# Optimization experiments

Hardware: AMD Instinct MI355X
Metric: run time of the kernel (lower is better)

## Reference

```python
import jax, jax.numpy as jnp
import numpy as np

N, E, D_IN, HID, HEADS, TS_OUT = 100000, 200000, 165, 64, 8, 5
HD1 = HID // HEADS  # 8 per-head channels in layer 1
HD2 = HID           # 64 per-head channels in layer 2 (concat=False -> mean)


def _glorot(key, shape):
    fan_in, fan_out = shape[0], shape[1]
    s = np.sqrt(6.0 / (fan_in + fan_out)).astype(np.float32)
    return jax.random.uniform(key, shape, jnp.float32, -s, s)


def setup_inputs() -> dict:
    key = jax.random.key(0)
    ks = jax.random.split(key, 24)
    inp = {
        "x": jax.random.normal(ks[0], (N, D_IN), jnp.float32),
        "edge_index": jax.random.randint(ks[1], (2, E), 0, N, jnp.int32),
        "timestamp_target": jax.random.randint(ks[2], (N,), 0, TS_OUT, jnp.int32),
        "node_target": jax.random.randint(ks[3], (N,), 0, 2, jnp.int32),
        "node_mask": jax.random.randint(ks[4], (N,), 0, 2, jnp.int32).astype(jnp.bool_),
        # GATConv layer 1: in=165 -> 8 heads x 8 ch, concat -> 64
        "W1": _glorot(ks[5], (D_IN, HEADS * HD1)),
        "att_src1": _glorot(ks[6], (HEADS, HD1)),
        "att_dst1": _glorot(ks[7], (HEADS, HD1)),
        "b1": jnp.zeros((HEADS * HD1,), jnp.float32),
        # GATConv layer 2: in=64 -> 8 heads x 64 ch, mean -> 64
        "W2": _glorot(ks[8], (HID, HEADS * HD2)),
        "att_src2": _glorot(ks[9], (HEADS, HD2)),
        "att_dst2": _glorot(ks[10], (HEADS, HD2)),
        "b2": jnp.zeros((HD2,), jnp.float32),
        # timestamp predictor MLP
        "ts_w1": _glorot(ks[11], (HID, HID)), "ts_b1": jnp.zeros((HID,), jnp.float32),
        "ts_w2": _glorot(ks[12], (HID, TS_OUT)), "ts_b2": jnp.zeros((TS_OUT,), jnp.float32),
        # class predictor MLP
        "cls_w1": _glorot(ks[13], (HID, HID)), "cls_b1": jnp.zeros((HID,), jnp.float32),
        "cls_w2": _glorot(ks[14], (HID, 2)), "cls_b2": jnp.zeros((2,), jnp.float32),
    }
    return inp


def _gat_layer(x, src, dst, n, W, a_src, a_dst, b, concat):
    H, C = a_src.shape
    h = (x @ W).reshape(n, H, C)                      # [N,H,C]
    a_s = (h * a_src).sum(-1)                         # [N,H]
    a_d = (h * a_dst).sum(-1)                         # [N,H]
    alpha = jax.nn.leaky_relu(a_s[src] + a_d[dst], 0.2)   # [E,H]
    amax = jax.ops.segment_max(alpha, dst, num_segments=n)
    ea = jnp.exp(alpha - amax[dst])
    denom = jax.ops.segment_sum(ea, dst, num_segments=n)
    a = ea / (denom[dst] + 1e-16)                     # segment softmax over incoming edges
    out = jax.ops.segment_sum(h[src] * a[:, :, None], dst, num_segments=n)  # [N,H,C]
    out = out.reshape(n, H * C) if concat else out.mean(axis=1)
    return out + b


def _ce(logits, targets):
    lp = jax.nn.log_softmax(logits, axis=-1)
    return -jnp.take_along_axis(lp, targets[:, None].astype(jnp.int32), axis=1)[:, 0]


def reference(x, edge_index, timestamp_target, node_target, node_mask,
              W1, att_src1, att_dst1, b1, W2, att_src2, att_dst2, b2,
              ts_w1, ts_b1, ts_w2, ts_b2, cls_w1, cls_b1, cls_w2, cls_b2):
    n = x.shape[0]
    loops = jnp.arange(n, dtype=edge_index.dtype)
    src = jnp.concatenate([edge_index[0], loops])     # add self loops (PyG default)
    dst = jnp.concatenate([edge_index[1], loops])
    h = _gat_layer(x, src, dst, n, W1, att_src1, att_dst1, b1, True)   # [N,64]
    h = _gat_layer(h, src, dst, n, W2, att_src2, att_dst2, b2, False)  # [N,64]
    # gradient reversal is identity in the forward pass
    ts_pred = jax.nn.relu(h @ ts_w1 + ts_b1) @ ts_w2 + ts_b2           # [N,5]
    cls_pred = jax.nn.relu(h @ cls_w1 + cls_b1) @ cls_w2 + cls_b2      # [N,2]
    ts_loss = _ce(ts_pred, timestamp_target).mean()
    m = node_mask.astype(jnp.float32)
    cls_loss = (_ce(cls_pred, node_target) * m).sum() / m.sum()
    return cls_loss + 1.0 * ts_loss
```

## Files before the change

kernel.cpp:

```cpp
#include <hip/hip_runtime.h>
#include <hip/hip_bf16.h>

#define NN 100000
#define NE 200000
#define NT (NE + NN)
#define DIN 165
#define PREPB 128
#define INITB 391
#define PACKB 32
#define W1PB 24
#define MISCGRID (PREPB + INITB + PACKB + W1PB)
#define NODEB 1563
#define XDW ((size_t)NN * DIN)
#define G1ROWS 32
#define G1NDMA 21

typedef __attribute__((ext_vector_type(8))) short bf16x8_t;
typedef __attribute__((ext_vector_type(4))) float f32x4_t;
typedef _Float16 h2_t __attribute__((ext_vector_type(2)));
typedef _Float16 f16x8_t __attribute__((ext_vector_type(8)));

#define AS1 __attribute__((address_space(1)))
#define AS3 __attribute__((address_space(3)))

static __device__ __forceinline__ unsigned short f2bf(float f) {
    __hip_bfloat16 b = __float2bfloat16(f);
    return *(unsigned short*)&b;
}
static __device__ __forceinline__ float bfu(unsigned short u) {
    __hip_bfloat16 b = *(__hip_bfloat16*)&u;
    return __bfloat162float(b);
}
static __device__ __forceinline__ unsigned pkh2(float a, float b) {
    h2_t v; v[0] = (_Float16)a; v[1] = (_Float16)b;
    return *(unsigned*)&v;
}


__global__ __launch_bounds__(256) void k_misc(const float* W2, const float* a2s, const float* a2d,
                                              float* wsd, __hip_bfloat16* W2pT,
                                              int* cnt, int* fill,
                                              const float* tsw1, const float* cw1,
                                              __hip_bfloat16* wB,
                                              const float* W1, unsigned* W1pT, float* zbuf) {
    int b = blockIdx.x;
    int tid = threadIdx.x;
    if (b < PREPB) {
        int i = b * 256 + tid;
        int c = i >> 9, j = i & 511;
        int hh = j >> 6, kk = j & 63;
        W2pT[i] = __float2bfloat16(W2[kk * 512 + hh * 64 + c]);
        if (b == 0) zbuf[tid] = 0.f;
        if (i < 512) {
            int h = i >> 6, k = i & 63;
            float s = 0.f, d = 0.f;
            for (int cc = 0; cc < 64; cc++) {
                float w = W2[k * 512 + h * 64 + cc];
                s += w * a2s[h * 64 + cc];
                d += w * a2d[h * 64 + cc];
            }
            wsd[i] = s; wsd[512 + i] = d;
        }
    } else if (b < PREPB + INITB) {
        int i = (b - PREPB) * 256 + tid;
        if (i < NN) { cnt[i] = 0; fill[i] = 0; }
    } else if (b < PREPB + INITB + PACKB) {
        int i = (b - PREPB - INITB) * 256 + tid;
        if (i < 8192) {
            int c = i >> 6, k = i & 63;
            float v = (c < 64) ? tsw1[k * 64 + c] : cw1[k * 64 + (c - 64)];
            wB[i] = __float2bfloat16(v);
        }
    } else {
        int i = (b - PREPB - INITB - PACKB) * 256 + tid;
        if (i < 6144) {
            int c = i / 96, kp = i - c * 96;
            int k = 2 * kp;
            float f0 = (k < DIN) ? W1[k * 64 + c] : 0.f;
            float f1 = (k + 1 < DIN) ? W1[(k + 1) * 64 + c] : 0.f;
            W1pT[i] = pkh2(f0, f1);
        }
    }
}


__global__ __launch_bounds__(256) void k_count(const int* dstE, int* cnt) {
    int e = blockIdx.x * 256 + threadIdx.x;
    if (e < NE) atomicAdd(&cnt[dstE[e]], 1);
}

__global__ __launch_bounds__(256) void k_scanA(const int* cnt, int* rowptr, int* bsum) {
    __shared__ int sm[256];
    int t = threadIdx.x;
    int base = blockIdx.x * 1024;
    int v[4]; int s = 0;
    for (int i = 0; i < 4; i++) {
        int idx = base + t * 4 + i;
        v[i] = (idx < NN) ? (cnt[idx] + 1) : 0;
        s += v[i];
    }
    sm[t] = s; __syncthreads();
    for (int off = 1; off < 256; off <<= 1) {
        int x = (t >= off) ? sm[t - off] : 0;
        __syncthreads();
        sm[t] += x;
        __syncthreads();
    }
    int run = sm[t] - s;
    for (int i = 0; i < 4; i++) {
        run += v[i];
        int idx = base + t * 4 + i;
        if (idx < NN) rowptr[idx + 1] = run;
    }
    if (t == 255) bsum[blockIdx.x] = sm[255];
}

__global__ __launch_bounds__(64) void k_scanB(int* bsum, int nb) {
    int lane = threadIdx.x;
    int v0 = (lane < nb) ? bsum[lane] : 0;
    int v1 = (64 + lane < nb) ? bsum[64 + lane] : 0;
    int s0 = v0;
    for (int off = 1; off < 64; off <<= 1) { int t = __shfl_up(s0, off); if (lane >= off) s0 += t; }
    int tot0 = __shfl(s0, 63);
    int s1 = v1;
    for (int off = 1; off < 64; off <<= 1) { int t = __shfl_up(s1, off); if (lane >= off) s1 += t; }
    if (lane < nb) bsum[lane] = s0 - v0;
    if (64 + lane < nb) bsum[64 + lane] = tot0 + s1 - v1;
}

__global__ __launch_bounds__(256) void k_scanC(const int* bsum, int* rowptr) {
    int i = blockIdx.x * 256 + threadIdx.x;
    if (i < NN) rowptr[i + 1] += bsum[i >> 10];
    if (i == 0) rowptr[0] = 0;
}

__global__ __launch_bounds__(256) void k_fill(const int* srcE, const int* dstE,
                                              const int* rowptr, int* fill, int* col, int* rowv) {
    int i = blockIdx.x * 256 + threadIdx.x;
    if (i >= NT) return;
    int s, d;
    if (i < NE) { s = srcE[i]; d = dstE[i]; }
    else        { s = i - NE; d = s; }
    int p = rowptr[d] + atomicAdd(&fill[d], 1);
    col[p] = s;
    rowv[p] = d;
}


__global__ __launch_bounds__(128) void k_gemm1(const float* x, const unsigned* W1pT,
                                               const float* att_s, const float* att_d,
                                               const float* zsrc,
                                               __hip_bfloat16* h1b, float* aad1) {
    __shared__ float X[G1NDMA * 256];
    int tid = threadIdx.x;
    int l = tid & 63, w = tid >> 6;
    int n0 = blockIdx.x * G1ROWS;
    int frow = l & 15, kg = l >> 4;

    size_t tb = (size_t)n0 * DIN;
    for (int i = w; i < G1NDMA; i += 2) {
        size_t gd = tb + (size_t)i * 256 + (size_t)l * 4;
        const float* g = (gd + 4 <= XDW) ? (x + gd) : (zsrc + l * 4);
        __builtin_amdgcn_global_load_lds((const AS1 float*)g,
                                         (AS3 float*)(X + i * 256), 16, 0, 0);
    }
    uint4 B[6][4];
    #pragma unroll
    for (int s = 0; s < 6; s++)
        #pragma unroll
        for (int t = 0; t < 4; t++)
            B[s][t] = *(const uint4*)&W1pT[(t * 16 + frow) * 96 + s * 16 + kg * 4];
    __syncthreads();

    f32x4_t acc[4] = {};
    int rbase = (w * 16 + frow) * DIN + kg * 8;
    #pragma unroll
    for (int s = 0; s < 6; s++) {
        f16x8_t av;
        #pragma unroll
        for (int j = 0; j < 8; j++) av[j] = (_Float16)X[rbase + s * 32 + j];
        #pragma unroll
        for (int t = 0; t < 4; t++)
            acc[t] = __builtin_amdgcn_mfma_f32_16x16x32_f16(av, *(f16x8_t*)&B[s][t], acc[t], 0, 0, 0);
    }

    int nw = n0 + w * 16;
    float asv[4], adv[4];
    #pragma unroll
    for (int t = 0; t < 4; t++) {
        int c = t * 16 + frow;
        asv[t] = att_s[c]; adv[t] = att_d[c];
    }
    int hb = (l >> 3) & 1;
    #pragma unroll
    for (int q = 0; q < 4; q++) {
        int n = nw + kg * 4 + q;
        #pragma unroll
        for (int t = 0; t < 4; t++) {
            float sv = acc[t][q] * asv[t];
            float dv = acc[t][q] * adv[t];
            sv += __shfl_xor(sv, 1); sv += __shfl_xor(sv, 2); sv += __shfl_xor(sv, 4);
            dv += __shfl_xor(dv, 1); dv += __shfl_xor(dv, 2); dv += __shfl_xor(dv, 4);
            if ((l & 7) == 0) {
                int h = t * 2 + hb;
                aad1[(size_t)n * 16 + h]     = sv;
                aad1[(size_t)n * 16 + 8 + h] = dv;
            }
        }
    }

    __syncthreads();
    unsigned short* Hw = (unsigned short*)X + w * 1152;
    #pragma unroll
    for (int t = 0; t < 4; t++)
        #pragma unroll
        for (int q = 0; q < 4; q++)
            Hw[(kg * 4 + q) * 72 + t * 16 + frow] = f2bf(acc[t][q]);
    int rr = l >> 2, cc = l & 3;
    int n2 = nw + rr;
    unsigned short* dst = (unsigned short*)h1b + (size_t)n2 * 64 + cc * 16;
    *(uint4*)dst       = *(const uint4*)&Hw[rr * 72 + cc * 16];
    *(uint4*)(dst + 8) = *(const uint4*)&Hw[rr * 72 + cc * 16 + 8];
}


__global__ __launch_bounds__(256) void k_edgew(const float* aad, const int* col, const int* rowv,
                                               __hip_bfloat16* web) {
    int e = blockIdx.x * 256 + threadIdx.x;
    if (e >= NT) return;
    int s = col[e], d = rowv[e];
    float4 s0 = *(const float4*)&aad[(size_t)s * 16];
    float4 s1 = *(const float4*)&aad[(size_t)s * 16 + 4];
    float4 dd0 = *(const float4*)&aad[(size_t)d * 16 + 8];
    float4 dd1 = *(const float4*)&aad[(size_t)d * 16 + 12];
    float as[8] = {s0.x, s0.y, s0.z, s0.w, s1.x, s1.y, s1.z, s1.w};
    float ad[8] = {dd0.x, dd0.y, dd0.z, dd0.w, dd1.x, dd1.y, dd1.z, dd1.w};
    unsigned p[4];
    #pragma unroll
    for (int q = 0; q < 4; q++) {
        float a0 = as[2*q]   + ad[2*q];
        float a1 = as[2*q+1] + ad[2*q+1];
        a0 = a0 > 0.f ? a0 : 0.2f * a0;
        a1 = a1 > 0.f ? a1 : 0.2f * a1;
        p[q] = (unsigned)f2bf(__expf(a0)) | ((unsigned)f2bf(__expf(a1)) << 16);
    }
    *(uint4*)&web[(size_t)e * 8] = make_uint4(p[0], p[1], p[2], p[3]);
}


__global__ __launch_bounds__(256) void k_agg1f(const __hip_bfloat16* h1b, const __hip_bfloat16* we1b,
                                               const int* rowptr, const int* col,
                                               const float* b1, const float* wsd,
                                               __hip_bfloat16* out1b, float* aad2) {
    int tid = threadIdx.x;
    int q8 = tid & 7;
    int n = blockIdx.x * 32 + (tid >> 3);
    const unsigned short* h1u = (const unsigned short*)h1b;
    const unsigned short* weu = (const unsigned short*)we1b;
    int rs = rowptr[n], re = rowptr[n + 1];
    float acc[8] = {};
    float den = 0.f;
    for (int eb = rs; eb < re; eb += 4) {
        int c4[4];
        #pragma unroll
        for (int j = 0; j < 4; j++) c4[j] = col[min(eb + j, re - 1)];
        #pragma unroll
        for (int j = 0; j < 4; j++) {
            int e = min(eb + j, re - 1);
            float w = bfu(weu[(size_t)e * 8 + q8]);
            w = (eb + j < re) ? w : 0.f;
            uint4 hv = *(const uint4*)&h1u[(size_t)c4[j] * 64 + q8 * 8];
            den += w;
            acc[0] += w * bfu((unsigned short)(hv.x & 0xffff));
            acc[1] += w * bfu((unsigned short)(hv.x >> 16));
            acc[2] += w * bfu((unsigned short)(hv.y & 0xffff));
            acc[3] += w * bfu((unsigned short)(hv.y >> 16));
            acc[4] += w * bfu((unsigned short)(hv.z & 0xffff));
            acc[5] += w * bfu((unsigned short)(hv.z >> 16));
            acc[6] += w * bfu((unsigned short)(hv.w & 0xffff));
            acc[7] += w * bfu((unsigned short)(hv.w >> 16));
        }
    }
    float inv = 1.0f / (den + 1e-16f);
    float4 b0 = *(const float4*)&b1[q8 * 8];
    float4 b4 = *(const float4*)&b1[q8 * 8 + 4];
    float bb[8] = {b0.x, b0.y, b0.z, b0.w, b4.x, b4.y, b4.z, b4.w};
    unsigned short u[8];
    float r[8];
    #pragma unroll
    for (int k = 0; k < 8; k++) {
        u[k] = f2bf(acc[k] * inv + bb[k]);
        r[k] = bfu(u[k]);
    }
    unsigned short* ou = (unsigned short*)out1b;
    uint4 pk;
    pk.x = (unsigned)u[0] | ((unsigned)u[1] << 16);
    pk.y = (unsigned)u[2] | ((unsigned)u[3] << 16);
    pk.z = (unsigned)u[4] | ((unsigned)u[5] << 16);
    pk.w = (unsigned)u[6] | ((unsigned)u[7] << 16);
    *(uint4*)&ou[(size_t)n * 64 + q8 * 8] = pk;

    float p[16];
    #pragma unroll
    for (int j = 0; j < 16; j++) {
        float4 w0 = *(const float4*)&wsd[j * 64 + q8 * 8];
        float4 w4 = *(const float4*)&wsd[j * 64 + q8 * 8 + 4];
        p[j] = r[0] * w0.x + r[1] * w0.y + r[2] * w0.z + r[3] * w0.w
             + r[4] * w4.x + r[5] * w4.y + r[6] * w4.z + r[7] * w4.w;
    }
    #pragma unroll
    for (int s = 1; s < 8; s <<= 1)
        #pragma unroll
        for (int j = 0; j < 16; j++) p[j] += __shfl_xor(p[j], s);
    float p0 = 0.f, p1 = 0.f;
    #pragma unroll
    for (int j = 0; j < 8; j++) {
        p0 = (q8 == j) ? p[j] : p0;
        p1 = (q8 == j) ? p[8 + j] : p1;
    }
    aad2[(size_t)n * 16 + q8]     = p0;
    aad2[(size_t)n * 16 + 8 + q8] = p1;
}


__global__ __launch_bounds__(256) void k_l2f(const __hip_bfloat16* out1b, const __hip_bfloat16* we2b,
                                             const int* rowptr, const int* col,
                                             const __hip_bfloat16* W2pT, const float* b2,
                                             const __hip_bfloat16* wB,
                                             const float* tsb1, const float* cb1,
                                             const float* tsw2, const float* tsb2,
                                             const float* cw2, const float* cb2,
                                             const int* tst, const int* ctg, const unsigned char* msk,
                                             float* part) {
    __shared__ unsigned short Ax[64 * 512];
    __shared__ unsigned short Bl[64 * 72];
    __shared__ float red[4][3];
    int tid = threadIdx.x;
    int l = tid & 63, w = tid >> 6;
    int n0 = blockIdx.x * 64;
    int frow = l & 15, kg = l >> 4;

    const unsigned short* o1u = (const unsigned short*)out1b;
    const unsigned short* weu = (const unsigned short*)we2b;
    int q8 = tid & 7;
    #pragma unroll 1
    for (int pass = 0; pass < 2; pass++) {
        int j = pass * 32 + (tid >> 3);
        int n = n0 + j;
        int rs = 0, re = 0;
        if (n < NN) { rs = rowptr[n]; re = rowptr[n + 1]; }
        float acc[8][8];
        float den[8];
        #pragma unroll
        for (int h = 0; h < 8; h++) {
            den[h] = 0.f;
            #pragma unroll
            for (int c = 0; c < 8; c++) acc[h][c] = 0.f;
        }
        for (int eb = rs; eb < re; eb += 4) {
            int c4[4];
            #pragma unroll
            for (int jj = 0; jj < 4; jj++) c4[jj] = col[min(eb + jj, re - 1)];
            #pragma unroll
            for (int jj = 0; jj < 4; jj++) {
                int e = min(eb + jj, re - 1);
                uint4 wv = *(const uint4*)&weu[(size_t)e * 8];
                uint4 hv = *(const uint4*)&o1u[(size_t)c4[jj] * 64 + q8 * 8];
                float vm = (eb + jj < re) ? 1.f : 0.f;
                float hc[8] = {bfu((unsigned short)(hv.x & 0xffff)), bfu((unsigned short)(hv.x >> 16)),
                               bfu((unsigned short)(hv.y & 0xffff)), bfu((unsigned short)(hv.y >> 16)),
                               bfu((unsigned short)(hv.z & 0xffff)), bfu((unsigned short)(hv.z >> 16)),
                               bfu((unsigned short)(hv.w & 0xffff)), bfu((unsigned short)(hv.w >> 16))};
                float wt[8] = {bfu((unsigned short)(wv.x & 0xffff)), bfu((unsigned short)(wv.x >> 16)),
                               bfu((unsigned short)(wv.y & 0xffff)), bfu((unsigned short)(wv.y >> 16)),
                               bfu((unsigned short)(wv.z & 0xffff)), bfu((unsigned short)(wv.z >> 16)),
                               bfu((unsigned short)(wv.w & 0xffff)), bfu((unsigned short)(wv.w >> 16))};
                #pragma unroll
                for (int h = 0; h < 8; h++) {
                    float ww = wt[h] * vm;
                    den[h] += ww;
                    #pragma unroll
                    for (int c = 0; c < 8; c++) acc[h][c] += ww * hc[c];
                }
            }
        }
        unsigned short* row = &Ax[j * 512];
        #pragma unroll
        for (int h = 0; h < 8; h++) {
            float inv = 1.0f / (den[h] + 1e-16f);
            uint4 pk;
            pk.x = (unsigned)f2bf(acc[h][0] * inv) | ((unsigned)f2bf(acc[h][1] * inv) << 16);
            pk.y = (unsigned)f2bf(acc[h][2] * inv) | ((unsigned)f2bf(acc[h][3] * inv) << 16);
            pk.z = (unsigned)f2bf(acc[h][4] * inv) | ((unsigned)f2bf(acc[h][5] * inv) << 16);
            pk.w = (unsigned)f2bf(acc[h][6] * inv) | ((unsigned)f2bf(acc[h][7] * inv) << 16);
            int blk = (h * 8 + q8) ^ (j & 7);
            *(uint4*)&row[blk * 8] = pk;
        }
    }
    __syncthreads();

    const unsigned short* B_g = (const unsigned short*)W2pT;
    f32x4_t gacc[4] = {};
    #pragma unroll 1
    for (int k0 = 0; k0 < 512; k0 += 64) {
        #pragma unroll
        for (int ll = 0; ll < 2; ll++) {
            int u = tid + ll * 256;
            int r = u >> 3, seg = u & 7;
            *(uint4*)&Bl[r * 72 + seg * 8] = *(const uint4*)&B_g[(size_t)r * 512 + k0 + seg * 8];
        }
        __syncthreads();
        #pragma unroll
        for (int kk = 0; kk < 2; kk++) {
            int blk = ((k0 >> 3) + kk * 4 + kg) ^ (frow & 7);
            bf16x8_t a = *(const bf16x8_t*)&Ax[(w * 16 + frow) * 512 + blk * 8];
            #pragma unroll
            for (int t = 0; t < 4; t++) {
                bf16x8_t bb = *(const bf16x8_t*)&Bl[(t * 16 + frow) * 72 + kk * 32 + kg * 8];
                gacc[t] = __builtin_amdgcn_mfma_f32_16x16x32_bf16(a, bb, gacc[t], 0, 0, 0);
            }
        }
        __syncthreads();
    }

    unsigned short* o2L = Ax;
    #pragma unroll
    for (int t = 0; t < 4; t++) {
        float bias = b2[t * 16 + frow];
        #pragma unroll
        for (int q = 0; q < 4; q++)
            o2L[(w * 16 + kg * 4 + q) * 72 + t * 16 + frow] = f2bf(0.125f * gacc[t][q] + bias);
    }
    __syncthreads();
    const unsigned short* wBu = (const unsigned short*)wB;
    f32x4_t a2c[8] = {};
    #pragma unroll
    for (int kk = 0; kk < 2; kk++) {
        bf16x8_t a2 = *(const bf16x8_t*)&o2L[(w * 16 + frow) * 72 + kk * 32 + kg * 8];
        #pragma unroll
        for (int t2 = 0; t2 < 8; t2++) {
            bf16x8_t b2f = *(const bf16x8_t*)&wBu[(t2 * 16 + frow) * 64 + kk * 32 + kg * 8];
            a2c[t2] = __builtin_amdgcn_mfma_f32_16x16x32_bf16(a2, b2f, a2c[t2], 0, 0, 0);
        }
    }

    float lg[4][5]; float lc[4][2];
    #pragma unroll
    for (int q = 0; q < 4; q++) {
        #pragma unroll
        for (int t = 0; t < 5; t++) lg[q][t] = 0.f;
        lc[q][0] = 0.f; lc[q][1] = 0.f;
    }
    #pragma unroll
    for (int t2 = 0; t2 < 4; t2++) {
        int c = t2 * 16 + frow;
        float bb = tsb1[c];
        float w0 = tsw2[c * 5 + 0], w1 = tsw2[c * 5 + 1], w2 = tsw2[c * 5 + 2],
              w3 = tsw2[c * 5 + 3], w4 = tsw2[c * 5 + 4];
        #pragma unroll
        for (int q = 0; q < 4; q++) {
            float v = fmaxf(a2c[t2][q] + bb, 0.f);
            lg[q][0] += v * w0; lg[q][1] += v * w1; lg[q][2] += v * w2;
            lg[q][3] += v * w3; lg[q][4] += v * w4;
        }
    }
    #pragma unroll
    for (int t2 = 0; t2 < 4; t2++) {
        int c = t2 * 16 + frow;
        float bb = cb1[c];
        float u0 = cw2[c * 2], u1 = cw2[c * 2 + 1];
        #pragma unroll
        for (int q = 0; q < 4; q++) {
            float v = fmaxf(a2c[t2 + 4][q] + bb, 0.f);
            lc[q][0] += v * u0; lc[q][1] += v * u1;
        }
    }
    #pragma unroll
    for (int q = 0; q < 4; q++) {
        #pragma unroll
        for (int t = 0; t < 5; t++) {
            lg[q][t] += __shfl_xor(lg[q][t], 1);
            lg[q][t] += __shfl_xor(lg[q][t], 2);
            lg[q][t] += __shfl_xor(lg[q][t], 4);
            lg[q][t] += __shfl_xor(lg[q][t], 8);
        }
        #pragma unroll
        for (int t = 0; t < 2; t++) {
            lc[q][t] += __shfl_xor(lc[q][t], 1);
            lc[q][t] += __shfl_xor(lc[q][t], 2);
            lc[q][t] += __shfl_xor(lc[q][t], 4);
            lc[q][t] += __shfl_xor(lc[q][t], 8);
        }
    }
    float tsl = 0.f, cll = 0.f, mval = 0.f;
    if (frow == 0) {
        #pragma unroll
        for (int q = 0; q < 4; q++) {
            int n = n0 + w * 16 + kg * 4 + q;
            if (n < NN) {
                float L[5];
                #pragma unroll
                for (int t = 0; t < 5; t++) L[t] = lg[q][t] + tsb2[t];
                float mx = fmaxf(fmaxf(fmaxf(L[0], L[1]), fmaxf(L[2], L[3])), L[4]);
                float se = 0.f;
                #pragma unroll
                for (int t = 0; t < 5; t++) se += __expf(L[t] - mx);
                int tg = tst[n];
                float pick = 0.f;
                #pragma unroll
                for (int t = 0; t < 5; t++) pick += (t == tg) ? L[t] : 0.f;
                tsl += mx + __logf(se) - pick;
                float C0 = lc[q][0] + cb2[0];
                float C1 = lc[q][1] + cb2[1];
                float mx2 = fmaxf(C0, C1);
                float lse2 = mx2 + __logf(__expf(C0 - mx2) + __expf(C1 - mx2));
                float mv = msk[n] ? 1.f : 0.f;
                float pick2 = ctg[n] ? C1 : C0;
                cll += (lse2 - pick2) * mv;
                mval += mv;
            }
        }
    }
    #pragma unroll
    for (int off = 1; off < 64; off <<= 1) {
        tsl  += __shfl_xor(tsl, off);
        cll  += __shfl_xor(cll, off);
        mval += __shfl_xor(mval, off);
    }
    if (l == 0) { red[w][0] = tsl; red[w][1] = cll; red[w][2] = mval; }
    __syncthreads();
    if (tid == 0) {
        part[blockIdx.x * 3 + 0] = red[0][0] + red[1][0] + red[2][0] + red[3][0];
        part[blockIdx.x * 3 + 1] = red[0][1] + red[1][1] + red[2][1] + red[3][1];
        part[blockIdx.x * 3 + 2] = red[0][2] + red[1][2] + red[2][2] + red[3][2];
    }
}

__global__ __launch_bounds__(256) void k_final(const float* part, float* out, int nb) {
    __shared__ float sm[3][256];
    int tid = threadIdx.x;
    float a = 0, b = 0, c = 0;
    for (int i = tid; i < nb; i += 256) { a += part[i*3]; b += part[i*3+1]; c += part[i*3+2]; }
    sm[0][tid] = a; sm[1][tid] = b; sm[2][tid] = c;
    __syncthreads();
    for (int s = 128; s > 0; s >>= 1) {
        if (tid < s) {
            sm[0][tid] += sm[0][tid + s];
            sm[1][tid] += sm[1][tid + s];
            sm[2][tid] += sm[2][tid + s];
        }
        __syncthreads();
    }
    if (tid == 0) out[0] = sm[1][0] / sm[2][0] + sm[0][0] / (float)NN;
}


extern "C" void kernel_launch(void* const* d_in, const int* in_sizes, int n_in,
                              void* d_out, int out_size, void* d_ws, size_t ws_size,
                              hipStream_t stream) {
    const float* x    = (const float*)d_in[0];
    const int*   ei   = (const int*)d_in[1];
    const int*   tst  = (const int*)d_in[2];
    const int*   ctg  = (const int*)d_in[3];
    const unsigned char* msk = (const unsigned char*)d_in[4];
    const float* W1   = (const float*)d_in[5];
    const float* a1s  = (const float*)d_in[6];
    const float* a1d  = (const float*)d_in[7];
    const float* b1   = (const float*)d_in[8];
    const float* W2   = (const float*)d_in[9];
    const float* a2s  = (const float*)d_in[10];
    const float* a2d  = (const float*)d_in[11];
    const float* b2   = (const float*)d_in[12];
    const float* tsw1 = (const float*)d_in[13];
    const float* tsb1 = (const float*)d_in[14];
    const float* tsw2 = (const float*)d_in[15];
    const float* tsb2 = (const float*)d_in[16];
    const float* cw1  = (const float*)d_in[17];
    const float* cb1  = (const float*)d_in[18];
    const float* cw2  = (const float*)d_in[19];
    const float* cb2  = (const float*)d_in[20];
    const int* srcE = ei;
    const int* dstE = ei + NE;

    char* ws = (char*)d_ws;
    size_t off = 0;
    auto alloc = [&](size_t b) { size_t o = off; off = (off + b + 255) & ~(size_t)255; return o; };
    int*   cnt    = (int*)(ws + alloc((size_t)NN * 4));
    int*   fill   = (int*)(ws + alloc((size_t)NN * 4));
    int*   rowptr = (int*)(ws + alloc((size_t)(NN + 1) * 4));
    int*   bsum   = (int*)(ws + alloc(128 * 4));
    int*   col    = (int*)(ws + alloc((size_t)NT * 4));
    int*   rowv   = (int*)(ws + alloc((size_t)NT * 4));
    float* aad1   = (float*)(ws + alloc((size_t)NN * 16 * 4));
    __hip_bfloat16* out1b = (__hip_bfloat16*)(ws + alloc((size_t)NN * 64 * 2));
    float* aad2   = (float*)(ws + alloc((size_t)NN * 16 * 4));
    float* wsd    = (float*)(ws + alloc(1024 * 4));
    __hip_bfloat16* W2pT  = (__hip_bfloat16*)(ws + alloc(32768 * 2));
    __hip_bfloat16* wB    = (__hip_bfloat16*)(ws + alloc(8192 * 2));
    unsigned* W1pT = (unsigned*)(ws + alloc(6144 * 4));
    float* zbuf   = (float*)(ws + alloc(256 * 4));
    __hip_bfloat16* h1b   = (__hip_bfloat16*)(ws + alloc((size_t)NN * 64 * 2));
    __hip_bfloat16* web   = (__hip_bfloat16*)(ws + alloc((size_t)NT * 8 * 2));
    float* part   = (float*)(ws + alloc((size_t)NODEB * 3 * 4));
    (void)ws_size; (void)in_sizes; (void)n_in; (void)out_size;

    int nb_scan = (NN + 1023) / 1024;

    k_misc<<<MISCGRID, 256, 0, stream>>>(W2, a2s, a2d, wsd, W2pT, cnt, fill,
                                         tsw1, cw1, wB, W1, W1pT, zbuf);
    k_count<<<(NE + 255) / 256, 256, 0, stream>>>(dstE, cnt);
    k_scanA<<<nb_scan, 256, 0, stream>>>(cnt, rowptr, bsum);
    k_scanB<<<1, 64, 0, stream>>>(bsum, nb_scan);
    k_scanC<<<(NN + 255) / 256, 256, 0, stream>>>(bsum, rowptr);
    k_fill<<<(NT + 255) / 256, 256, 0, stream>>>(srcE, dstE, rowptr, fill, col, rowv);

    k_gemm1<<<NN / G1ROWS, 128, 0, stream>>>(x, W1pT, a1s, a1d, zbuf, h1b, aad1);
    k_edgew<<<(NT + 255) / 256, 256, 0, stream>>>(aad1, col, rowv, web);
    k_agg1f<<<NN / 32, 256, 0, stream>>>(h1b, web, rowptr, col, b1, wsd, out1b, aad2);
    k_edgew<<<(NT + 255) / 256, 256, 0, stream>>>(aad2, col, rowv, web);

    k_l2f<<<NODEB, 256, 0, stream>>>(out1b, web, rowptr, col, W2pT, b2, wB,
                                     tsb1, cb1, tsw2, tsb2, cw2, cb2, tst, ctg, msk, part);

    k_final<<<1, 256, 0, stream>>>(part, (float*)d_out, NODEB);
}
```

Measured before the change: 177.7 us.

## Fuse edge-weight computation into aggregation kernels and drop scan and final launches

Removes the two k_edgew passes and computes the leaky-relu/exp attention weights inline inside both aggregation kernels, reading per-node attention scalars from aad instead of a materialized per-edge bf16 weight array. The weights are now fp32 rather than bf16-rounded. Merges k_scanB into k_scanC, where every block recomputes the block prefix in shared memory, and replaces k_final with atomic accumulation plus a last-block-done finish in k_l2f. This cuts four launches and the per-edge weight write/read traffic, at the cost of redundant exp work per lane and wave shuffles in layer 2.

```diff
diff --git a/kernel.cpp b/kernel.cpp
--- a/kernel.cpp
+++ b/kernel.cpp
@@ -42,7 +42,8 @@
                                               int* cnt, int* fill,
                                               const float* tsw1, const float* cw1,
                                               __hip_bfloat16* wB,
-                                              const float* W1, unsigned* W1pT, float* zbuf) {
+                                              const float* W1, unsigned* W1pT, float* zbuf,
+                                              float* acc3, int* cnt1) {
     int b = blockIdx.x;
     int tid = threadIdx.x;
     if (b < PREPB) {
@@ -51,6 +52,7 @@
         int hh = j >> 6, kk = j & 63;
         W2pT[i] = __float2bfloat16(W2[kk * 512 + hh * 64 + c]);
         if (b == 0) zbuf[tid] = 0.f;
+        if (b == 0 && tid == 0) { acc3[0] = 0.f; acc3[1] = 0.f; acc3[2] = 0.f; cnt1[0] = 0; }
         if (i < 512) {
             int h = i >> 6, k = i & 63;
             float s = 0.f, d = 0.f;
@@ -115,22 +117,24 @@
     if (t == 255) bsum[blockIdx.x] = sm[255];
 }
 
-__global__ __launch_bounds__(64) void k_scanB(int* bsum, int nb) {
-    int lane = threadIdx.x;
-    int v0 = (lane < nb) ? bsum[lane] : 0;
-    int v1 = (64 + lane < nb) ? bsum[64 + lane] : 0;
-    int s0 = v0;
-    for (int off = 1; off < 64; off <<= 1) { int t = __shfl_up(s0, off); if (lane >= off) s0 += t; }
-    int tot0 = __shfl(s0, 63);
-    int s1 = v1;
-    for (int off = 1; off < 64; off <<= 1) { int t = __shfl_up(s1, off); if (lane >= off) s1 += t; }
-    if (lane < nb) bsum[lane] = s0 - v0;
-    if (64 + lane < nb) bsum[64 + lane] = tot0 + s1 - v1;
-}
-
-__global__ __launch_bounds__(256) void k_scanC(const int* bsum, int* rowptr) {
-    int i = blockIdx.x * 256 + threadIdx.x;
-    if (i < NN) rowptr[i + 1] += bsum[i >> 10];
+__global__ __launch_bounds__(256) void k_scanC(const int* bsum, int* rowptr, int nb) {
+    __shared__ int pre[128];
+    int tid = threadIdx.x;
+    if (tid < 64) {
+        int lane = tid;
+        int v0 = (lane < nb) ? bsum[lane] : 0;
+        int v1 = (64 + lane < nb) ? bsum[64 + lane] : 0;
+        int s0 = v0;
+        for (int off = 1; off < 64; off <<= 1) { int t = __shfl_up(s0, off); if (lane >= off) s0 += t; }
+        int tot0 = __shfl(s0, 63);
+        int s1 = v1;
+        for (int off = 1; off < 64; off <<= 1) { int t = __shfl_up(s1, off); if (lane >= off) s1 += t; }
+        pre[lane] = s0 - v0;
+        pre[64 + lane] = tot0 + s1 - v1;
+    }
+    __syncthreads();
+    int i = blockIdx.x * 256 + tid;
+    if (i < NN) rowptr[i + 1] += pre[i >> 10];
     if (i == 0) rowptr[0] = 0;
 }
 
@@ -224,31 +228,7 @@
 }
 
 
-__global__ __launch_bounds__(256) void k_edgew(const float* aad, const int* col, const int* rowv,
-                                               __hip_bfloat16* web) {
-    int e = blockIdx.x * 256 + threadIdx.x;
-    if (e >= NT) return;
-    int s = col[e], d = rowv[e];
-    float4 s0 = *(const float4*)&aad[(size_t)s * 16];
-    float4 s1 = *(const float4*)&aad[(size_t)s * 16 + 4];
-    float4 dd0 = *(const float4*)&aad[(size_t)d * 16 + 8];
-    float4 dd1 = *(const float4*)&aad[(size_t)d * 16 + 12];
-    float as[8] = {s0.x, s0.y, s0.z, s0.w, s1.x, s1.y, s1.z, s1.w};
-    float ad[8] = {dd0.x, dd0.y, dd0.z, dd0.w, dd1.x, dd1.y, dd1.z, dd1.w};
-    unsigned p[4];
-    #pragma unroll
-    for (int q = 0; q < 4; q++) {
-        float a0 = as[2*q]   + ad[2*q];
-        float a1 = as[2*q+1] + ad[2*q+1];
-        a0 = a0 > 0.f ? a0 : 0.2f * a0;
-        a1 = a1 > 0.f ? a1 : 0.2f * a1;
-        p[q] = (unsigned)f2bf(__expf(a0)) | ((unsigned)f2bf(__expf(a1)) << 16);
-    }
-    *(uint4*)&web[(size_t)e * 8] = make_uint4(p[0], p[1], p[2], p[3]);
-}
-
-
-__global__ __launch_bounds__(256) void k_agg1f(const __hip_bfloat16* h1b, const __hip_bfloat16* we1b,
+__global__ __launch_bounds__(256) void k_agg1f(const __hip_bfloat16* h1b, const float* aad1,
                                                const int* rowptr, const int* col,
                                                const float* b1, const float* wsd,
                                                __hip_bfloat16* out1b, float* aad2) {
@@ -256,7 +236,7 @@
     int q8 = tid & 7;
     int n = blockIdx.x * 32 + (tid >> 3);
     const unsigned short* h1u = (const unsigned short*)h1b;
-    const unsigned short* weu = (const unsigned short*)we1b;
+    float ad_own = aad1[(size_t)n * 16 + 8 + q8];
     int rs = rowptr[n], re = rowptr[n + 1];
     float acc[8] = {};
     float den = 0.f;
@@ -264,12 +244,19 @@
         int c4[4];
         #pragma unroll
         for (int j = 0; j < 4; j++) c4[j] = col[min(eb + j, re - 1)];
+        float asv[4]; uint4 hv4[4];
         #pragma unroll
         for (int j = 0; j < 4; j++) {
-            int e = min(eb + j, re - 1);
-            float w = bfu(weu[(size_t)e * 8 + q8]);
+            asv[j] = aad1[(size_t)c4[j] * 16 + q8];
+            hv4[j] = *(const uint4*)&h1u[(size_t)c4[j] * 64 + q8 * 8];
+        }
+        #pragma unroll
+        for (int j = 0; j < 4; j++) {
+            float a = asv[j] + ad_own;
+            a = a > 0.f ? a : 0.2f * a;
+            float w = __expf(a);
             w = (eb + j < re) ? w : 0.f;
-            uint4 hv = *(const uint4*)&h1u[(size_t)c4[j] * 64 + q8 * 8];
+            uint4 hv = hv4[j];
             den += w;
             acc[0] += w * bfu((unsigned short)(hv.x & 0xffff));
             acc[1] += w * bfu((unsigned short)(hv.x >> 16));
@@ -323,7 +310,7 @@
 }
 
 
-__global__ __launch_bounds__(256) void k_l2f(const __hip_bfloat16* out1b, const __hip_bfloat16* we2b,
+__global__ __launch_bounds__(256) void k_l2f(const __hip_bfloat16* out1b, const float* aad2,
                                              const int* rowptr, const int* col,
                                              const __hip_bfloat16* W2pT, const float* b2,
                                              const __hip_bfloat16* wB,
@@ -331,7 +318,7 @@
                                              const float* tsw2, const float* tsb2,
                                              const float* cw2, const float* cb2,
                                              const int* tst, const int* ctg, const unsigned char* msk,
-                                             float* part) {
+                                             float* acc3, int* cnt1, float* out) {
     __shared__ unsigned short Ax[64 * 512];
     __shared__ unsigned short Bl[64 * 72];
     __shared__ float red[4][3];
@@ -341,14 +328,18 @@
     int frow = l & 15, kg = l >> 4;
 
     const unsigned short* o1u = (const unsigned short*)out1b;
-    const unsigned short* weu = (const unsigned short*)we2b;
     int q8 = tid & 7;
+    int base8 = l & 56;
     #pragma unroll 1
     for (int pass = 0; pass < 2; pass++) {
         int j = pass * 32 + (tid >> 3);
         int n = n0 + j;
         int rs = 0, re = 0;
-        if (n < NN) { rs = rowptr[n]; re = rowptr[n + 1]; }
+        float ad_own = 0.f;
+        if (n < NN) {
+            rs = rowptr[n]; re = rowptr[n + 1];
+            ad_own = aad2[(size_t)n * 16 + 8 + q8];
+        }
         float acc[8][8];
         float den[8];
         #pragma unroll
@@ -361,26 +352,31 @@
             int c4[4];
             #pragma unroll
             for (int jj = 0; jj < 4; jj++) c4[jj] = col[min(eb + jj, re - 1)];
+            float asv[4]; uint4 hv4[4];
             #pragma unroll
             for (int jj = 0; jj < 4; jj++) {
-                int e = min(eb + jj, re - 1);
-                uint4 wv = *(const uint4*)&weu[(size_t)e * 8];
-                uint4 hv = *(const uint4*)&o1u[(size_t)c4[jj] * 64 + q8 * 8];
-                float vm = (eb + jj < re) ? 1.f : 0.f;
+                asv[jj] = aad2[(size_t)c4[jj] * 16 + q8];
+                hv4[jj] = *(const uint4*)&o1u[(size_t)c4[jj] * 64 + q8 * 8];
+            }
+            #pragma unroll
+            for (int jj = 0; jj < 4; jj++) {
+                float a = asv[jj] + ad_own;
+                a = a > 0.f ? a : 0.2f * a;
+                float wq = __expf(a);
+                wq = (eb + jj < re) ? wq : 0.f;
+                float wt[8];
+                #pragma unroll
+                for (int h = 0; h < 8; h++) wt[h] = __shfl(wq, base8 + h);
+                uint4 hv = hv4[jj];
                 float hc[8] = {bfu((unsigned short)(hv.x & 0xffff)), bfu((unsigned short)(hv.x >> 16)),
                                bfu((unsigned short)(hv.y & 0xffff)), bfu((unsigned short)(hv.y >> 16)),
                                bfu((unsigned short)(hv.z & 0xffff)), bfu((unsigned short)(hv.z >> 16)),
                                bfu((unsigned short)(hv.w & 0xffff)), bfu((unsigned short)(hv.w >> 16))};
-                float wt[8] = {bfu((unsigned short)(wv.x & 0xffff)), bfu((unsigned short)(wv.x >> 16)),
-                               bfu((unsigned short)(wv.y & 0xffff)), bfu((unsigned short)(wv.y >> 16)),
-                               bfu((unsigned short)(wv.z & 0xffff)), bfu((unsigned short)(wv.z >> 16)),
-                               bfu((unsigned short)(wv.w & 0xffff)), bfu((unsigned short)(wv.w >> 16))};
                 #pragma unroll
                 for (int h = 0; h < 8; h++) {
-                    float ww = wt[h] * vm;
-                    den[h] += ww;
+                    den[h] += wt[h];
                     #pragma unroll
-                    for (int c = 0; c < 8; c++) acc[h][c] += ww * hc[c];
+                    for (int c = 0; c < 8; c++) acc[h][c] += wt[h] * hc[c];
                 }
             }
         }
@@ -530,28 +526,21 @@
     if (l == 0) { red[w][0] = tsl; red[w][1] = cll; red[w][2] = mval; }
     __syncthreads();
     if (tid == 0) {
-        part[blockIdx.x * 3 + 0] = red[0][0] + red[1][0] + red[2][0] + red[3][0];
-        part[blockIdx.x * 3 + 1] = red[0][1] + red[1][1] + red[2][1] + red[3][1];
-        part[blockIdx.x * 3 + 2] = red[0][2] + red[1][2] + red[2][2] + red[3][2];
-    }
-}
-
-__global__ __launch_bounds__(256) void k_final(const float* part, float* out, int nb) {
-    __shared__ float sm[3][256];
-    int tid = threadIdx.x;
-    float a = 0, b = 0, c = 0;
-    for (int i = tid; i < nb; i += 256) { a += part[i*3]; b += part[i*3+1]; c += part[i*3+2]; }
-    sm[0][tid] = a; sm[1][tid] = b; sm[2][tid] = c;
-    __syncthreads();
-    for (int s = 128; s > 0; s >>= 1) {
-        if (tid < s) {
-            sm[0][tid] += sm[0][tid + s];
-            sm[1][tid] += sm[1][tid + s];
-            sm[2][tid] += sm[2][tid + s];
-        }
-        __syncthreads();
-    }
-    if (tid == 0) out[0] = sm[1][0] / sm[2][0] + sm[0][0] / (float)NN;
+        float s0 = red[0][0] + red[1][0] + red[2][0] + red[3][0];
+        float s1 = red[0][1] + red[1][1] + red[2][1] + red[3][1];
+        float s2 = red[0][2] + red[1][2] + red[2][2] + red[3][2];
+        atomicAdd(&acc3[0], s0);
+        atomicAdd(&acc3[1], s1);
+        atomicAdd(&acc3[2], s2);
+        __threadfence();
+        int old = atomicAdd(cnt1, 1);
+        if (old == NODEB - 1) {
+            float t0 = atomicAdd(&acc3[0], 0.f);
+            float t1 = atomicAdd(&acc3[1], 0.f);
+            float t2 = atomicAdd(&acc3[2], 0.f);
+            out[0] = t1 / t2 + t0 / (float)NN;
+        }
+    }
 }
 
 
@@ -600,27 +589,23 @@
     unsigned* W1pT = (unsigned*)(ws + alloc(6144 * 4));
     float* zbuf   = (float*)(ws + alloc(256 * 4));
     __hip_bfloat16* h1b   = (__hip_bfloat16*)(ws + alloc((size_t)NN * 64 * 2));
-    __hip_bfloat16* web   = (__hip_bfloat16*)(ws + alloc((size_t)NT * 8 * 2));
-    float* part   = (float*)(ws + alloc((size_t)NODEB * 3 * 4));
+    float* acc3   = (float*)(ws + alloc(4 * 4));
+    int*   cnt1   = (int*)(ws + alloc(4 * 4));
     (void)ws_size; (void)in_sizes; (void)n_in; (void)out_size;
 
     int nb_scan = (NN + 1023) / 1024;
 
     k_misc<<<MISCGRID, 256, 0, stream>>>(W2, a2s, a2d, wsd, W2pT, cnt, fill,
-                                         tsw1, cw1, wB, W1, W1pT, zbuf);
+                                         tsw1, cw1, wB, W1, W1pT, zbuf, acc3, cnt1);
     k_count<<<(NE + 255) / 256, 256, 0, stream>>>(dstE, cnt);
     k_scanA<<<nb_scan, 256, 0, stream>>>(cnt, rowptr, bsum);
-    k_scanB<<<1, 64, 0, stream>>>(bsum, nb_scan);
-    k_scanC<<<(NN + 255) / 256, 256, 0, stream>>>(bsum, rowptr);
+    k_scanC<<<(NN + 255) / 256, 256, 0, stream>>>(bsum, rowptr, nb_scan);
     k_fill<<<(NT + 255) / 256, 256, 0, stream>>>(srcE, dstE, rowptr, fill, col, rowv);
 
     k_gemm1<<<NN / G1ROWS, 128, 0, stream>>>(x, W1pT, a1s, a1d, zbuf, h1b, aad1);
-    k_edgew<<<(NT + 255) / 256, 256, 0, stream>>>(aad1, col, rowv, web);
-    k_agg1f<<<NN / 32, 256, 0, stream>>>(h1b, web, rowptr, col, b1, wsd, out1b, aad2);
-    k_edgew<<<(NT + 255) / 256, 256, 0, stream>>>(aad2, col, rowv, web);
-
-    k_l2f<<<NODEB, 256, 0, stream>>>(out1b, web, rowptr, col, W2pT, b2, wB,
-                                     tsb1, cb1, tsw2, tsb2, cw2, cb2, tst, ctg, msk, part);
-
-    k_final<<<1, 256, 0, stream>>>(part, (float*)d_out, NODEB);
-}
+    k_agg1f<<<NN / 32, 256, 0, stream>>>(h1b, aad1, rowptr, col, b1, wsd, out1b, aad2);
+
+    k_l2f<<<NODEB, 256, 0, stream>>>(out1b, aad2, rowptr, col, W2pT, b2, wB,
+                                     tsb1, cb1, tsw2, tsb2, cw2, cb2, tst, ctg, msk,
+                                     acc3, cnt1, (float*)d_out);
+}
```

Result: slower. 208.6 us (+17.4%).

## Halve layer-2 node tile, fold final reduction and scan into fewer launches

Applied to the files above, without the earlier changes.

The fused layer-2 kernel now handles 32 nodes per block instead of 64, with 3125 blocks, and its MFMA work is redistributed across the four waves (each wave takes a 16x32 output tile, and ts/cls heads are split between wave pairs). The separate final reduction kernel is replaced by atomic accumulation plus a last-block-done counter, and the block-sum scan kernel is merged into the scan-add kernel. This removes two kernel launches and the per-block serial two-pass loop, and the smaller LDS footprint should raise occupancy. The cost is float atomics with nondeterministic summation order and each scanC block redundantly scanning the block sums.

```diff
diff --git a/kernel.cpp b/kernel.cpp
--- a/kernel.cpp
+++ b/kernel.cpp
@@ -10,7 +10,7 @@
 #define PACKB 32
 #define W1PB 24
 #define MISCGRID (PREPB + INITB + PACKB + W1PB)
-#define NODEB 1563
+#define L2B 3125
 #define XDW ((size_t)NN * DIN)
 #define G1ROWS 32
 #define G1NDMA 21
@@ -42,7 +42,8 @@
                                               int* cnt, int* fill,
                                               const float* tsw1, const float* cw1,
                                               __hip_bfloat16* wB,
-                                              const float* W1, unsigned* W1pT, float* zbuf) {
+                                              const float* W1, unsigned* W1pT, float* zbuf,
+                                              float* acc3, int* cnt1) {
     int b = blockIdx.x;
     int tid = threadIdx.x;
     if (b < PREPB) {
@@ -51,6 +52,7 @@
         int hh = j >> 6, kk = j & 63;
         W2pT[i] = __float2bfloat16(W2[kk * 512 + hh * 64 + c]);
         if (b == 0) zbuf[tid] = 0.f;
+        if (b == 0 && tid == 0) { acc3[0] = 0.f; acc3[1] = 0.f; acc3[2] = 0.f; cnt1[0] = 0; }
         if (i < 512) {
             int h = i >> 6, k = i & 63;
             float s = 0.f, d = 0.f;
@@ -115,22 +117,24 @@
     if (t == 255) bsum[blockIdx.x] = sm[255];
 }
 
-__global__ __launch_bounds__(64) void k_scanB(int* bsum, int nb) {
-    int lane = threadIdx.x;
-    int v0 = (lane < nb) ? bsum[lane] : 0;
-    int v1 = (64 + lane < nb) ? bsum[64 + lane] : 0;
-    int s0 = v0;
-    for (int off = 1; off < 64; off <<= 1) { int t = __shfl_up(s0, off); if (lane >= off) s0 += t; }
-    int tot0 = __shfl(s0, 63);
-    int s1 = v1;
-    for (int off = 1; off < 64; off <<= 1) { int t = __shfl_up(s1, off); if (lane >= off) s1 += t; }
-    if (lane < nb) bsum[lane] = s0 - v0;
-    if (64 + lane < nb) bsum[64 + lane] = tot0 + s1 - v1;
-}
-
-__global__ __launch_bounds__(256) void k_scanC(const int* bsum, int* rowptr) {
-    int i = blockIdx.x * 256 + threadIdx.x;
-    if (i < NN) rowptr[i + 1] += bsum[i >> 10];
+__global__ __launch_bounds__(256) void k_scanC(const int* bsum, int* rowptr, int nb) {
+    __shared__ int pre[128];
+    int tid = threadIdx.x;
+    if (tid < 64) {
+        int lane = tid;
+        int v0 = (lane < nb) ? bsum[lane] : 0;
+        int v1 = (64 + lane < nb) ? bsum[64 + lane] : 0;
+        int s0 = v0;
+        for (int off = 1; off < 64; off <<= 1) { int t = __shfl_up(s0, off); if (lane >= off) s0 += t; }
+        int tot0 = __shfl(s0, 63);
+        int s1 = v1;
+        for (int off = 1; off < 64; off <<= 1) { int t = __shfl_up(s1, off); if (lane >= off) s1 += t; }
+        pre[lane] = s0 - v0;
+        pre[64 + lane] = tot0 + s1 - v1;
+    }
+    __syncthreads();
+    int i = blockIdx.x * 256 + tid;
+    if (i < NN) rowptr[i + 1] += pre[i >> 10];
     if (i == 0) rowptr[0] = 0;
 }
 
@@ -331,24 +335,22 @@
                                              const float* tsw2, const float* tsb2,
                                              const float* cw2, const float* cb2,
                                              const int* tst, const int* ctg, const unsigned char* msk,
-                                             float* part) {
-    __shared__ unsigned short Ax[64 * 512];
+                                             float* acc3, int* cnt1, float* out) {
+    __shared__ unsigned short Ax[32 * 512];
     __shared__ unsigned short Bl[64 * 72];
     __shared__ float red[4][3];
     int tid = threadIdx.x;
     int l = tid & 63, w = tid >> 6;
-    int n0 = blockIdx.x * 64;
+    int n0 = blockIdx.x * 32;
     int frow = l & 15, kg = l >> 4;
 
     const unsigned short* o1u = (const unsigned short*)out1b;
     const unsigned short* weu = (const unsigned short*)we2b;
     int q8 = tid & 7;
-    #pragma unroll 1
-    for (int pass = 0; pass < 2; pass++) {
-        int j = pass * 32 + (tid >> 3);
+    {
+        int j = tid >> 3;
         int n = n0 + j;
-        int rs = 0, re = 0;
-        if (n < NN) { rs = rowptr[n]; re = rowptr[n + 1]; }
+        int rs = rowptr[n], re = rowptr[n + 1];
         float acc[8][8];
         float den[8];
         #pragma unroll
@@ -400,7 +402,9 @@
     __syncthreads();
 
     const unsigned short* B_g = (const unsigned short*)W2pT;
-    f32x4_t gacc[4] = {};
+    int r0 = (w & 1) * 16;
+    int c0 = (w >> 1) * 32;
+    f32x4_t gacc[2] = {};
     #pragma unroll 1
     for (int k0 = 0; k0 < 512; k0 += 64) {
         #pragma unroll
@@ -413,10 +417,10 @@
         #pragma unroll
         for (int kk = 0; kk < 2; kk++) {
             int blk = ((k0 >> 3) + kk * 4 + kg) ^ (frow & 7);
-            bf16x8_t a = *(const bf16x8_t*)&Ax[(w * 16 + frow) * 512 + blk * 8];
-            #pragma unroll
-            for (int t = 0; t < 4; t++) {
-                bf16x8_t bb = *(const bf16x8_t*)&Bl[(t * 16 + frow) * 72 + kk * 32 + kg * 8];
+            bf16x8_t a = *(const bf16x8_t*)&Ax[(r0 + frow) * 512 + blk * 8];
+            #pragma unroll
+            for (int t = 0; t < 2; t++) {
+                bf16x8_t bb = *(const bf16x8_t*)&Bl[(c0 + t * 16 + frow) * 72 + kk * 32 + kg * 8];
                 gacc[t] = __builtin_amdgcn_mfma_f32_16x16x32_bf16(a, bb, gacc[t], 0, 0, 0);
             }
         }
@@ -425,79 +429,61 @@
 
     unsigned short* o2L = Ax;
     #pragma unroll
-    for (int t = 0; t < 4; t++) {
-        float bias = b2[t * 16 + frow];
+    for (int t = 0; t < 2; t++) {
+        float bias = b2[c0 + t * 16 + frow];
+        f32x4_t g = gacc[t];
         #pragma unroll
         for (int q = 0; q < 4; q++)
-            o2L[(w * 16 + kg * 4 + q) * 72 + t * 16 + frow] = f2bf(0.125f * gacc[t][q] + bias);
+            o2L[(r0 + kg * 4 + q) * 72 + c0 + t * 16 + frow] = f2bf(0.125f * g[q] + bias);
     }
     __syncthreads();
     const unsigned short* wBu = (const unsigned short*)wB;
-    f32x4_t a2c[8] = {};
+    int m0 = (w & 1) * 16;
+    int h0 = (w >> 1) * 64;
+    f32x4_t a2c[4] = {};
     #pragma unroll
     for (int kk = 0; kk < 2; kk++) {
-        bf16x8_t a2 = *(const bf16x8_t*)&o2L[(w * 16 + frow) * 72 + kk * 32 + kg * 8];
-        #pragma unroll
-        for (int t2 = 0; t2 < 8; t2++) {
-            bf16x8_t b2f = *(const bf16x8_t*)&wBu[(t2 * 16 + frow) * 64 + kk * 32 + kg * 8];
-            a2c[t2] = __builtin_amdgcn_mfma_f32_16x16x32_bf16(a2, b2f, a2c[t2], 0, 0, 0);
-        }
-    }
-
-    float lg[4][5]; float lc[4][2];
-    #pragma unroll
-    for (int q = 0; q < 4; q++) {
-        #pragma unroll
-        for (int t = 0; t < 5; t++) lg[q][t] = 0.f;
-        lc[q][0] = 0.f; lc[q][1] = 0.f;
-    }
-    #pragma unroll
-    for (int t2 = 0; t2 < 4; t2++) {
-        int c = t2 * 16 + frow;
-        float bb = tsb1[c];
-        float w0 = tsw2[c * 5 + 0], w1 = tsw2[c * 5 + 1], w2 = tsw2[c * 5 + 2],
-              w3 = tsw2[c * 5 + 3], w4 = tsw2[c * 5 + 4];
-        #pragma unroll
-        for (int q = 0; q < 4; q++) {
-            float v = fmaxf(a2c[t2][q] + bb, 0.f);
-            lg[q][0] += v * w0; lg[q][1] += v * w1; lg[q][2] += v * w2;
-            lg[q][3] += v * w3; lg[q][4] += v * w4;
-        }
-    }
-    #pragma unroll
-    for (int t2 = 0; t2 < 4; t2++) {
-        int c = t2 * 16 + frow;
-        float bb = cb1[c];
-        float u0 = cw2[c * 2], u1 = cw2[c * 2 + 1];
-        #pragma unroll
-        for (int q = 0; q < 4; q++) {
-            float v = fmaxf(a2c[t2 + 4][q] + bb, 0.f);
-            lc[q][0] += v * u0; lc[q][1] += v * u1;
-        }
-    }
-    #pragma unroll
-    for (int q = 0; q < 4; q++) {
-        #pragma unroll
-        for (int t = 0; t < 5; t++) {
-            lg[q][t] += __shfl_xor(lg[q][t], 1);
-            lg[q][t] += __shfl_xor(lg[q][t], 2);
-            lg[q][t] += __shfl_xor(lg[q][t], 4);
-            lg[q][t] += __shfl_xor(lg[q][t], 8);
-        }
-        #pragma unroll
-        for (int t = 0; t < 2; t++) {
-            lc[q][t] += __shfl_xor(lc[q][t], 1);
-            lc[q][t] += __shfl_xor(lc[q][t], 2);
-            lc[q][t] += __shfl_xor(lc[q][t], 4);
-            lc[q][t] += __shfl_xor(lc[q][t], 8);
-        }
-    }
+        bf16x8_t a2 = *(const bf16x8_t*)&o2L[(m0 + frow) * 72 + kk * 32 + kg * 8];
+        #pragma unroll
+        for (int t2 = 0; t2 < 4; t2++) {
+            bf16x8_t bf = *(const bf16x8_t*)&wBu[(h0 + t2 * 16 + frow) * 64 + kk * 32 + kg * 8];
+            a2c[t2] = __builtin_amdgcn_mfma_f32_16x16x32_bf16(a2, bf, a2c[t2], 0, 0, 0);
+        }
+    }
+
     float tsl = 0.f, cll = 0.f, mval = 0.f;
-    if (frow == 0) {
-        #pragma unroll
-        for (int q = 0; q < 4; q++) {
-            int n = n0 + w * 16 + kg * 4 + q;
-            if (n < NN) {
+    if ((w >> 1) == 0) {
+        float lg[4][5];
+        #pragma unroll
+        for (int q = 0; q < 4; q++)
+            #pragma unroll
+            for (int t = 0; t < 5; t++) lg[q][t] = 0.f;
+        #pragma unroll
+        for (int t2 = 0; t2 < 4; t2++) {
+            int c = t2 * 16 + frow;
+            float bb = tsb1[c];
+            float w0 = tsw2[c * 5 + 0], w1 = tsw2[c * 5 + 1], w2 = tsw2[c * 5 + 2],
+                  w3 = tsw2[c * 5 + 3], w4 = tsw2[c * 5 + 4];
+            #pragma unroll
+            for (int q = 0; q < 4; q++) {
+                float v = fmaxf(a2c[t2][q] + bb, 0.f);
+                lg[q][0] += v * w0; lg[q][1] += v * w1; lg[q][2] += v * w2;
+                lg[q][3] += v * w3; lg[q][4] += v * w4;
+            }
+        }
+        #pragma unroll
+        for (int q = 0; q < 4; q++)
+            #pragma unroll
+            for (int t = 0; t < 5; t++) {
+                lg[q][t] += __shfl_xor(lg[q][t], 1);
+                lg[q][t] += __shfl_xor(lg[q][t], 2);
+                lg[q][t] += __shfl_xor(lg[q][t], 4);
+                lg[q][t] += __shfl_xor(lg[q][t], 8);
+            }
+        if (frow == 0) {
+            #pragma unroll
+            for (int q = 0; q < 4; q++) {
+                int n = n0 + m0 + kg * 4 + q;
                 float L[5];
                 #pragma unroll
                 for (int t = 0; t < 5; t++) L[t] = lg[q][t] + tsb2[t];
@@ -510,6 +496,36 @@
                 #pragma unroll
                 for (int t = 0; t < 5; t++) pick += (t == tg) ? L[t] : 0.f;
                 tsl += mx + __logf(se) - pick;
+            }
+        }
+    } else {
+        float lc[4][2];
+        #pragma unroll
+        for (int q = 0; q < 4; q++) { lc[q][0] = 0.f; lc[q][1] = 0.f; }
+        #pragma unroll
+        for (int t2 = 0; t2 < 4; t2++) {
+            int c = t2 * 16 + frow;
+            float bb = cb1[c];
+            float u0 = cw2[c * 2], u1 = cw2[c * 2 + 1];
+            #pragma unroll
+            for (int q = 0; q < 4; q++) {
+                float v = fmaxf(a2c[t2][q] + bb, 0.f);
+                lc[q][0] += v * u0; lc[q][1] += v * u1;
+            }
+        }
+        #pragma unroll
+        for (int q = 0; q < 4; q++)
+            #pragma unroll
+            for (int t = 0; t < 2; t++) {
+                lc[q][t] += __shfl_xor(lc[q][t], 1);
+                lc[q][t] += __shfl_xor(lc[q][t], 2);
+                lc[q][t] += __shfl_xor(lc[q][t], 4);
+                lc[q][t] += __shfl_xor(lc[q][t], 8);
+            }
+        if (frow == 0) {
+            #pragma unroll
+            for (int q = 0; q < 4; q++) {
+                int n = n0 + m0 + kg * 4 + q;
                 float C0 = lc[q][0] + cb2[0];
                 float C1 = lc[q][1] + cb2[1];
                 float mx2 = fmaxf(C0, C1);
@@ -530,28 +546,21 @@
     if (l == 0) { red[w][0] = tsl; red[w][1] = cll; red[w][2] = mval; }
     __syncthreads();
     if (tid == 0) {
-        part[blockIdx.x * 3 + 0] = red[0][0] + red[1][0] + red[2][0] + red[3][0];
-        part[blockIdx.x * 3 + 1] = red[0][1] + red[1][1] + red[2][1] + red[3][1];
-        part[blockIdx.x * 3 + 2] = red[0][2] + red[1][2] + red[2][2] + red[3][2];
-    }
-}
-
-__global__ __launch_bounds__(256) void k_final(const float* part, float* out, int nb) {
-    __shared__ float sm[3][256];
-    int tid = threadIdx.x;
-    float a = 0, b = 0, c = 0;
-    for (int i = tid; i < nb; i += 256) { a += part[i*3]; b += part[i*3+1]; c += part[i*3+2]; }
-    sm[0][tid] = a; sm[1][tid] = b; sm[2][tid] = c;
-    __syncthreads();
-    for (int s = 128; s > 0; s >>= 1) {
-        if (tid < s) {
-            sm[0][tid] += sm[0][tid + s];
-            sm[1][tid] += sm[1][tid + s];
-            sm[2][tid] += sm[2][tid + s];
-        }
-        __syncthreads();
-    }
-    if (tid == 0) out[0] = sm[1][0] / sm[2][0] + sm[0][0] / (float)NN;
+        float s0 = red[0][0] + red[1][0] + red[2][0] + red[3][0];
+        float s1 = red[0][1] + red[1][1] + red[2][1] + red[3][1];
+        float s2 = red[0][2] + red[1][2] + red[2][2] + red[3][2];
+        atomicAdd(&acc3[0], s0);
+        atomicAdd(&acc3[1], s1);
+        atomicAdd(&acc3[2], s2);
+        __threadfence();
+        int old = atomicAdd(cnt1, 1);
+        if (old == L2B - 1) {
+            float t0 = atomicAdd(&acc3[0], 0.f);
+            float t1 = atomicAdd(&acc3[1], 0.f);
+            float t2 = atomicAdd(&acc3[2], 0.f);
+            out[0] = t1 / t2 + t0 / (float)NN;
+        }
+    }
 }
 
 
@@ -601,17 +610,17 @@
     float* zbuf   = (float*)(ws + alloc(256 * 4));
     __hip_bfloat16* h1b   = (__hip_bfloat16*)(ws + alloc((size_t)NN * 64 * 2));
     __hip_bfloat16* web   = (__hip_bfloat16*)(ws + alloc((size_t)NT * 8 * 2));
-    float* part   = (float*)(ws + alloc((size_t)NODEB * 3 * 4));
+    float* acc3   = (float*)(ws + alloc(4 * 4));
+    int*   cnt1   = (int*)(ws + alloc(4 * 4));
     (void)ws_size; (void)in_sizes; (void)n_in; (void)out_size;
 
     int nb_scan = (NN + 1023) / 1024;
 
     k_misc<<<MISCGRID, 256, 0, stream>>>(W2, a2s, a2d, wsd, W2pT, cnt, fill,
-                                         tsw1, cw1, wB, W1, W1pT, zbuf);
+                                         tsw1, cw1, wB, W1, W1pT, zbuf, acc3, cnt1);
     k_count<<<(NE + 255) / 256, 256, 0, stream>>>(dstE, cnt);
     k_scanA<<<nb_scan, 256, 0, stream>>>(cnt, rowptr, bsum);
-    k_scanB<<<1, 64, 0, stream>>>(bsum, nb_scan);
-    k_scanC<<<(NN + 255) / 256, 256, 0, stream>>>(bsum, rowptr);
+    k_scanC<<<(NN + 255) / 256, 256, 0, stream>>>(bsum, rowptr, nb_scan);
     k_fill<<<(NT + 255) / 256, 256, 0, stream>>>(srcE, dstE, rowptr, fill, col, rowv);
 
     k_gemm1<<<NN / G1ROWS, 128, 0, stream>>>(x, W1pT, a1s, a1d, zbuf, h1b, aad1);
@@ -619,8 +628,7 @@
     k_agg1f<<<NN / 32, 256, 0, stream>>>(h1b, web, rowptr, col, b1, wsd, out1b, aad2);
     k_edgew<<<(NT + 255) / 256, 256, 0, stream>>>(aad2, col, rowv, web);
 
-    k_l2f<<<NODEB, 256, 0, stream>>>(out1b, web, rowptr, col, W2pT, b2, wB,
-                                     tsb1, cb1, tsw2, tsb2, cw2, cb2, tst, ctg, msk, part);
-
-    k_final<<<1, 256, 0, stream>>>(part, (float*)d_out, NODEB);
-}
+    k_l2f<<<L2B, 256, 0, stream>>>(out1b, web, rowptr, col, W2pT, b2, wB,
+                                   tsb1, cb1, tsw2, tsb2, cw2, cb2, tst, ctg, msk,
+                                   acc3, cnt1, (float*)d_out);
+}
```

Result: slower. 252.9 us (+42.3%).
